# Optimization experiments

Measured on AMD Instinct MI355X. Metric: run time of the kernel, lower is better.

Reference implementation:

```python
import math
import jax, jax.numpy as jnp
from jax import lax
import numpy as np

B, S, D = 4, 128, 256          # batch, image side (l_max = S*S), d_model
FO = 64                        # filter_order (MLP width)
EMB = 3                        # emb_dim (time + 1 band sine/cosine)
FAST, SLOW, TARGET = 0.3, 1.5, 0.01


def setup_inputs() -> dict:
    key = jax.random.key(0)
    ks = jax.random.split(key, 20)
    d3 = 3 * D
    def rn(k, shp, scale):
        return jax.random.normal(k, shp, jnp.float32) * scale
    inp = {
        "x": jax.random.normal(ks[0], (B, S * S, D), jnp.float32),
        # in_proj / out_proj
        "in_w": rn(ks[1], (D, d3), 1.0 / math.sqrt(D)),
        "in_b": jnp.zeros((d3,), jnp.float32),
        "out_w": rn(ks[2], (D, D), 1.0 / math.sqrt(D)),
        "out_b": jnp.zeros((D,), jnp.float32),
        # depthwise 3x3 short filter
        "sf_w": rn(ks[3], (d3, 1, 3, 3), 1.0 / 3.0),
        "sf_b": jnp.zeros((d3,), jnp.float32),
        # Sin activation frequency (shared across all Sin uses; w=1, train_freq=True)
        "freq": jnp.ones((1, FO), jnp.float32),
        # X implicit filter MLP: Linear(3,FO) -> Sin -> Linear(FO,FO) -> Sin -> Linear(FO,FO) -> Sin -> Linear(FO,D,no bias)
        "xw0": rn(ks[4], (EMB, FO), 0.5), "xb0": jnp.zeros((FO,), jnp.float32),
        "xw1": rn(ks[5], (FO, FO), 1.0 / math.sqrt(FO)), "xb1": jnp.zeros((FO,), jnp.float32),
        "xw2": rn(ks[6], (FO, FO), 1.0 / math.sqrt(FO)), "xb2": jnp.zeros((FO,), jnp.float32),
        "xw3": rn(ks[7], (FO, D), 1.0 / math.sqrt(FO)),
        # Y implicit filter MLP (same structure)
        "yw0": rn(ks[8], (EMB, FO), 0.5), "yb0": jnp.zeros((FO,), jnp.float32),
        "yw1": rn(ks[9], (FO, FO), 1.0 / math.sqrt(FO)), "yb1": jnp.zeros((FO,), jnp.float32),
        "yw2": rn(ks[10], (FO, FO), 1.0 / math.sqrt(FO)), "yb2": jnp.zeros((FO,), jnp.float32),
        "yw3": rn(ks[11], (FO, D), 1.0 / math.sqrt(FO)),
        # HyenaFilter2d residual bias D (torch: randn)
        "fbias": jax.random.normal(ks[12], (D,), jnp.float32),
    }
    return inp


def _pos_emb():
    # PositionalEmbedding with emb_dim=3 -> bands=1
    t = jnp.linspace(0.0, 1.0, S)[None, :, None]                 # (1,S,1)
    tr = jnp.linspace(0.0, S - 1.0, S)[None, :, None]
    w_ang = 2.0 * math.pi * tr / S
    f = jnp.linspace(1e-4, 0.0, 1)[None, None]                   # bands=1
    zc = jnp.exp(-1j * f * w_ang)                                # (1,S,1) complex
    z = jnp.concatenate([t, zc.real, zc.imag], axis=-1)          # (1,S,3)
    return z.astype(jnp.float32), t.astype(jnp.float32)


def _decay(t):
    max_d = math.log(TARGET) / FAST
    min_d = math.log(TARGET) / SLOW
    deltas = jnp.linspace(min_d, max_d, D)[None, None]           # (1,1,D) buffer
    return jnp.exp(-t * jnp.abs(deltas))                         # (1,S,D)


def _mlp(z, freq, w0, b0, w1, b1, w2, b2, w3):
    h = jnp.sin(freq * (z @ w0 + b0))
    h = jnp.sin(freq * (h @ w1 + b1))
    h = jnp.sin(freq * (h @ w2 + b2))
    return h @ w3                                                # (1,S,D)


def _fftconv2d(u, k, Db):
    # u: (B,D,S,S), k: (D,S,S), Db: (D,)
    n = 2 * S
    kf = jnp.fft.rfft2(k.astype(jnp.float32), s=(n, n)) / n
    uf = jnp.fft.rfft2(u.astype(jnp.float32), s=(n, n))
    y = jnp.fft.irfft2(uf * kf, s=(n, n))[..., :S, :S]
    return y + u * Db[None, :, None, None]


def reference(x, in_w, in_b, out_w, out_b, sf_w, sf_b, freq,
              xw0, xb0, xw1, xb1, xw2, xb2, xw3,
              yw0, yb0, yw1, yb1, yw2, yb2, yw3, fbias):
    d3 = 3 * D
    # projection and reshape to 2D grid: b (h w) c -> b c h w
    u = x @ in_w + in_b                                          # (B,L,3D)
    u = u.reshape(B, S, S, d3).transpose(0, 3, 1, 2)             # (B,3D,S,S)
    # depthwise 3x3 short filter, padding=2, crop to S (matches Conv padding=2 + [:S])
    uc = lax.conv_general_dilated(u, sf_w, (1, 1), ((2, 2), (2, 2)),
                                  feature_group_count=d3,
                                  dimension_numbers=("NCHW", "OIHW", "NCHW"))
    uc = uc[..., :S, :S] + sf_b[None, :, None, None]
    x0, x1, v = jnp.split(uc, 3, axis=1)                         # each (B,D,S,S)
    # implicit separable 2D filter
    z, t = _pos_emb()
    dec = _decay(t)
    hx = _mlp(z, freq, xw0, xb0, xw1, xb1, xw2, xb2, xw3) * dec  # (1,S,D)
    hy = _mlp(z, freq, yw0, yb0, yw1, yb1, yw2, yb2, yw3) * dec
    k = jnp.einsum('ijk,imk->ijmk', hx, hy)[0]                   # (S,S,D)
    k = jnp.transpose(k, (2, 0, 1))                              # (D,S,S)
    # hyena recurrence (order=2): single gated fft conv
    v = v * x1
    v = _fftconv2d(v, k, fbias)
    y = v * x0
    y = y.transpose(0, 2, 3, 1).reshape(B, S * S, D)             # b c h w -> b (h w) c
    return y @ out_w + out_b
```

## Files before the change

### kernel.cpp

```cpp
#include <hip/hip_runtime.h>
#include <hip/hip_bf16.h>

#define S_DIM 128
#define B_DIM 4
#define L_DIM (S_DIM * S_DIM)

typedef __bf16 bf16x8 __attribute__((ext_vector_type(8)));
typedef float f32x4 __attribute__((ext_vector_type(4)));

__device__ __forceinline__ float b2f(unsigned short u) {
    union { unsigned int i; float f; } v;
    v.i = ((unsigned int)u) << 16;
    return v.f;
}
__device__ __forceinline__ unsigned short f2b(float f) {
    union { float f; unsigned int i; } v;
    v.f = f;
    unsigned int x = v.i;
    return (unsigned short)((x + 0x7FFFu + ((x >> 16) & 1u)) >> 16);
}
__device__ __forceinline__ float ldx(const void* p, size_t i, int f32) {
    return f32 ? ((const float*)p)[i] : b2f(((const unsigned short*)p)[i]);
}

__global__ __launch_bounds__(256) void sniff_dtype(const unsigned short* __restrict__ x,
                                                   int* __restrict__ flag) {
    __shared__ int cnt;
    if (threadIdx.x == 0) cnt = 0;
    __syncthreads();
    int c = 0;
    for (int i = threadIdx.x; i < 32768; i += 256) {
        unsigned int e = (x[i] >> 7) & 0xFFu;
        if (e >= 0x91u) c++;
    }
    atomicAdd(&cnt, c);
    __syncthreads();
    if (threadIdx.x == 0) flag[0] = (cnt > 64) ? 1 : 0;
}

__global__ void transpose_any(const void* __restrict__ src,
                              unsigned short* __restrict__ dst, int R, int C,
                              const int* __restrict__ flag) {
    const int f = flag[0];
    int idx = blockIdx.x * 256 + threadIdx.x;
    if (idx >= R * C) return;
    int r = idx / C, c = idx - r * C;
    dst[c * R + r] = f2b(ldx(src, idx, f));
}

__global__ __launch_bounds__(256) void cast_to_bf16(
    const void* __restrict__ src, size_t s_off,
    unsigned short* __restrict__ dst, size_t n,
    const int* __restrict__ flag)
{
    const int f = flag[0];
    size_t idx = ((size_t)blockIdx.x * 256 + threadIdx.x) * 8;
    const size_t stride = (size_t)gridDim.x * 256 * 8;
    for (; idx < n; idx += stride) {
        if (f) {
            const float4* s4 = (const float4*)((const float*)src + s_off + idx);
            float4 a = s4[0], b = s4[1];
            uint4 w;
            w.x = (unsigned int)f2b(a.x) | ((unsigned int)f2b(a.y) << 16);
            w.y = (unsigned int)f2b(a.z) | ((unsigned int)f2b(a.w) << 16);
            w.z = (unsigned int)f2b(b.x) | ((unsigned int)f2b(b.y) << 16);
            w.w = (unsigned int)f2b(b.z) | ((unsigned int)f2b(b.w) << 16);
            *(uint4*)(dst + idx) = w;
        } else {
            *(uint4*)(dst + idx) =
                *(const uint4*)((const unsigned short*)src + s_off + idx);
        }
    }
}

__global__ __launch_bounds__(256) void filter_mlp(
    const void* __restrict__ freq,
    const void* __restrict__ w0, const void* __restrict__ b0,
    const void* __restrict__ w1, const void* __restrict__ b1,
    const void* __restrict__ w2, const void* __restrict__ b2,
    const void* __restrict__ w3,
    float* __restrict__ out, const int* __restrict__ flag)
{
    __shared__ float hs[64], gs[64];
    const int f32f = flag[0];
    const int s   = blockIdx.x;
    const int tid = threadIdx.x;
    const float t = (float)s / (float)(S_DIM - 1);
    const float ang = 1e-4f * 2.0f * 3.14159265358979323846f * ((float)s / (float)S_DIM);
    const float z0 = t, z1 = cosf(ang), z2 = -sinf(ang);

    if (tid < 64) {
        float fr = ldx(freq, tid, f32f);
        float a = z0 * ldx(w0, 0 * 64 + tid, f32f) + z1 * ldx(w0, 1 * 64 + tid, f32f) +
                  z2 * ldx(w0, 2 * 64 + tid, f32f) + ldx(b0, tid, f32f);
        hs[tid] = sinf(fr * a);
    }
    __syncthreads();
    if (tid < 64) {
        float fr = ldx(freq, tid, f32f);
        float a = ldx(b1, tid, f32f);
        for (int e = 0; e < 64; e++) a += hs[e] * ldx(w1, e * 64 + tid, f32f);
        gs[tid] = sinf(fr * a);
    }
    __syncthreads();
    if (tid < 64) {
        float fr = ldx(freq, tid, f32f);
        float a = ldx(b2, tid, f32f);
        for (int e = 0; e < 64; e++) a += gs[e] * ldx(w2, e * 64 + tid, f32f);
        hs[tid] = sinf(fr * a);
    }
    __syncthreads();
    {
        const float min_d = -3.0701134573253943f;
        const float max_d = -15.350567286626971f;
        float a = 0.f;
        for (int e = 0; e < 64; e++) a += hs[e] * ldx(w3, e * 256 + tid, f32f);
        float delta = min_d + (max_d - min_d) * ((float)tid / 255.0f);
        float dec = expf(-t * fabsf(delta));
        out[s * 256 + tid] = a * dec;
    }
}

__global__ __launch_bounds__(256) void gemm_bt(
    const void* __restrict__ A, size_t a_off, int a_ext,
    const unsigned short* __restrict__ BT,
    const void* __restrict__ bias, int bias_ext,
    void* __restrict__ C, size_t c_off, int c_ext,
    int M, int N, int K, const int* __restrict__ flag)
{
    __shared__ unsigned short As[128 * 40];
    __shared__ unsigned short Bs[128 * 40];

    const int f     = flag[0];
    const int a_f32 = a_ext && f;
    const int b_f32 = bias_ext && f;
    const int c_f32 = c_ext && f;

    const int tid  = threadIdx.x;
    const int m0   = blockIdx.x * 128;
    const int n0   = blockIdx.y * 128;
    const int wid  = tid >> 6;
    const int lane = tid & 63;
    const int lrow = lane & 15;
    const int quad = lane >> 4;
    const int wr   = wid >> 1, wc = wid & 1;

    f32x4 acc[4][4];
#pragma unroll
    for (int a = 0; a < 4; a++)
#pragma unroll
        for (int b = 0; b < 4; b++)
#pragma unroll
            for (int r = 0; r < 4; r++) acc[a][b][r] = 0.0f;

    for (int kc = 0; kc < K; kc += 32) {
#pragma unroll
        for (int h = 0; h < 2; h++) {
            int c    = tid + h * 256;
            int row  = c >> 2;
            int col8 = (c & 3) * 8;
            size_t aidx = a_off + (size_t)(m0 + row) * K + kc + col8;
            if (a_f32) {
                const float4* ga = (const float4*)((const float*)A + aidx);
                float4 p0 = ga[0], p1 = ga[1];
                uint4 w;
                w.x = (unsigned int)f2b(p0.x) | ((unsigned int)f2b(p0.y) << 16);
                w.y = (unsigned int)f2b(p0.z) | ((unsigned int)f2b(p0.w) << 16);
                w.z = (unsigned int)f2b(p1.x) | ((unsigned int)f2b(p1.y) << 16);
                w.w = (unsigned int)f2b(p1.z) | ((unsigned int)f2b(p1.w) << 16);
                *(uint4*)(&As[row * 40 + col8]) = w;
            } else {
                *(uint4*)(&As[row * 40 + col8]) =
                    *(const uint4*)((const unsigned short*)A + aidx);
            }
            *(uint4*)(&Bs[row * 40 + col8]) =
                *(const uint4*)(BT + (size_t)(n0 + row) * K + kc + col8);
        }
        __syncthreads();

        bf16x8 af[4], bfr[4];
#pragma unroll
        for (int fm = 0; fm < 4; fm++)
            af[fm] = *(const bf16x8*)(&As[(wr * 64 + fm * 16 + lrow) * 40 + quad * 8]);
#pragma unroll
        for (int fn = 0; fn < 4; fn++)
            bfr[fn] = *(const bf16x8*)(&Bs[(wc * 64 + fn * 16 + lrow) * 40 + quad * 8]);
#pragma unroll
        for (int fm = 0; fm < 4; fm++)
#pragma unroll
            for (int fn = 0; fn < 4; fn++)
                acc[fm][fn] = __builtin_amdgcn_mfma_f32_16x16x32_bf16(
                    af[fm], bfr[fn], acc[fm][fn], 0, 0, 0);
        __syncthreads();
    }

#pragma unroll
    for (int fm = 0; fm < 4; fm++) {
#pragma unroll
        for (int fn = 0; fn < 4; fn++) {
            int gcol = n0 + wc * 64 + fn * 16 + lrow;
            float bv = ldx(bias, gcol, b_f32);
#pragma unroll
            for (int r = 0; r < 4; r++) {
                int grow = m0 + wr * 64 + fm * 16 + quad * 4 + r;
                size_t cidx = c_off + (size_t)grow * N + gcol;
                float val = acc[fm][fn][r] + bv;
                if (c_f32) ((float*)C)[cidx] = val;
                else       ((unsigned short*)C)[cidx] = f2b(val);
            }
        }
    }
}

__global__ __launch_bounds__(192) void conv3_gate(
    const unsigned short* __restrict__ U, size_t u_zs,
    const void* __restrict__ sfw, const void* __restrict__ sfb,
    unsigned short* __restrict__ Wb, unsigned short* __restrict__ X0, size_t o_zs,
    const int* __restrict__ flag)
{
    __shared__ __align__(16) float x1f[2][256];

    const int f32f = flag[0];
    const int i    = blockIdx.x;
    const int j0   = blockIdx.y * 32;
    const int tid  = threadIdx.x;
    const int wv   = tid >> 6;
    const int lane = tid & 63;
    const int ch0  = wv * 256 + lane * 4;

    const unsigned short* Ub = U + (size_t)blockIdx.z * u_zs;
    unsigned short* Wbb = Wb + (size_t)blockIdx.z * o_zs;
    unsigned short* X0b = X0 + (size_t)blockIdx.z * o_zs;

    float wgt[3][3][4], bias[4];
#pragma unroll
    for (int c = 0; c < 4; c++) {
        int ch = ch0 + c;
        bias[c] = ldx(sfb, ch, f32f);
#pragma unroll
        for (int ki = 0; ki < 3; ki++)
#pragma unroll
            for (int kj = 0; kj < 3; kj++)
                wgt[ki][kj][c] = ldx(sfw, ch * 9 + ki * 3 + kj, f32f);
    }

    bool rok[3];
    const unsigned short* rp[3];
#pragma unroll
    for (int ki = 0; ki < 3; ki++) {
        int row = i + ki - 2;
        rok[ki] = (row >= 0);
        rp[ki]  = Ub + (size_t)(row * S_DIM) * 768 + ch0;
    }

    float win[3][3][4];
#define DLOAD(slot, col)                                                       \
    { _Pragma("unroll") for (int ki = 0; ki < 3; ki++) {                       \
        if (rok[ki] && (col) >= 0) {                                           \
            uint2 p = *(const uint2*)(rp[ki] + (size_t)(col) * 768);           \
            win[slot][ki][0] = b2f((unsigned short)p.x);                       \
            win[slot][ki][1] = b2f((unsigned short)(p.x >> 16));               \
            win[slot][ki][2] = b2f((unsigned short)p.y);                       \
            win[slot][ki][3] = b2f((unsigned short)(p.y >> 16));               \
        } else {                                                               \
            win[slot][ki][0] = 0.f; win[slot][ki][1] = 0.f;                    \
            win[slot][ki][2] = 0.f; win[slot][ki][3] = 0.f;                    \
        } } }

    DLOAD(0, j0 - 2)
    DLOAD(1, j0 - 1)

    uint2 nxt[3];
#pragma unroll
    for (int ki = 0; ki < 3; ki++) {
        uint2 p; p.x = 0u; p.y = 0u;
        if (rok[ki]) p = *(const uint2*)(rp[ki] + (size_t)j0 * 768);
        nxt[ki] = p;
    }

#pragma unroll
    for (int jj = 0; jj < 32; jj++) {
        const int j  = j0 + jj;
        const int sA = jj % 3, sB = (jj + 1) % 3, sC = (jj + 2) % 3;

#pragma unroll
        for (int ki = 0; ki < 3; ki++) {
            win[sC][ki][0] = b2f((unsigned short)nxt[ki].x);
            win[sC][ki][1] = b2f((unsigned short)(nxt[ki].x >> 16));
            win[sC][ki][2] = b2f((unsigned short)nxt[ki].y);
            win[sC][ki][3] = b2f((unsigned short)(nxt[ki].y >> 16));
        }
        {
            const int jn = j + 1;
            const bool jok = (jn < S_DIM);
#pragma unroll
            for (int ki = 0; ki < 3; ki++) {
                uint2 p; p.x = 0u; p.y = 0u;
                if (jok && rok[ki]) p = *(const uint2*)(rp[ki] + (size_t)jn * 768);
                nxt[ki] = p;
            }
        }

        float o[4];
#pragma unroll
        for (int c = 0; c < 4; c++) {
            float a = bias[c];
#pragma unroll
            for (int ki = 0; ki < 3; ki++)
                a += wgt[ki][0][c] * win[sA][ki][c]
                   + wgt[ki][1][c] * win[sB][ki][c]
                   + wgt[ki][2][c] * win[sC][ki][c];
            o[c] = a;
        }

        const size_t oidx = (size_t)(i * S_DIM + j) * 256 + lane * 4;
        if (wv == 1) {
            float4 v4; v4.x = o[0]; v4.y = o[1]; v4.z = o[2]; v4.w = o[3];
            *(float4*)(&x1f[jj & 1][lane * 4]) = v4;
        } else if (wv == 0) {
            unsigned int lo = (unsigned int)f2b(o[0]) | ((unsigned int)f2b(o[1]) << 16);
            unsigned int hi = (unsigned int)f2b(o[2]) | ((unsigned int)f2b(o[3]) << 16);
            uint2 st; st.x = lo; st.y = hi;
            *(uint2*)(&X0b[oidx]) = st;
        }
        __syncthreads();
        if (wv == 2) {
            float4 xp = *(const float4*)(&x1f[jj & 1][lane * 4]);
            float r0 = o[0] * xp.x;
            float r1 = o[1] * xp.y;
            float r2 = o[2] * xp.z;
            float r3 = o[3] * xp.w;
            unsigned int lo = (unsigned int)f2b(r0) | ((unsigned int)f2b(r1) << 16);
            unsigned int hi = (unsigned int)f2b(r2) | ((unsigned int)f2b(r3) << 16);
            uint2 st; st.x = lo; st.y = hi;
            *(uint2*)(&Wbb[oidx]) = st;
        }
    }
#undef DLOAD
}

__global__ __launch_bounds__(256) void conv_j(
    const unsigned short* __restrict__ Wb, size_t zs,
    const float* __restrict__ hy,
    unsigned short* __restrict__ Aout)
{
    const int i = blockIdx.x;
    const int h = blockIdx.y;
    const int d = threadIdx.x;
    const size_t zoff = (size_t)blockIdx.z * zs;
    const size_t sbase = zoff + (size_t)(i * S_DIM) * 256;
    const unsigned short* Wp = Wb + sbase + d;
    const float* hyd = hy + d;

    for (int pick = 0; pick < 2; pick++) {
        const int jt = pick ? (7 - h) : h;
        const int j0 = jt * 16;
        float acc[16];
#pragma unroll
        for (int jj = 0; jj < 16; jj++) acc[jj] = 0.f;

        float Wn[19];
#pragma unroll
        for (int t = 0; t < 19; t++) {
            int r = j0 - 3 + t;
            Wn[t] = (r >= 0) ? b2f(Wp[(size_t)r * 256]) : 0.f;
        }
        const int qmax = j0 + 15;
        float hvA[4], hvB[4];
#pragma unroll
        for (int idx = 0; idx < 4; idx++) hvA[idx] = hyd[idx * 256];

        for (int q0 = 0; q0 <= qmax; q0 += 8) {
#pragma unroll
            for (int idx = 0; idx < 4; idx++) hvB[idx] = hyd[(q0 + 4 + idx) * 256];
#pragma unroll
            for (int idx = 0; idx < 4; idx++)
#pragma unroll
                for (int jj = 0; jj < 16; jj++)
                    acc[jj] += hvA[idx] * Wn[jj + 3 - idx];
#pragma unroll
            for (int t = 18; t >= 4; t--) Wn[t] = Wn[t - 4];
#pragma unroll
            for (int t = 0; t < 4; t++) {
                int r = j0 - q0 - 7 + t;
                Wn[t] = (r >= 0) ? b2f(Wp[(size_t)r * 256]) : 0.f;
            }
            if (q0 + 8 <= qmax) {
#pragma unroll
                for (int idx = 0; idx < 4; idx++) hvA[idx] = hyd[(q0 + 8 + idx) * 256];
            }
#pragma unroll
            for (int idx = 0; idx < 4; idx++)
#pragma unroll
                for (int jj = 0; jj < 16; jj++)
                    acc[jj] += hvB[idx] * Wn[jj + 3 - idx];
            if (q0 + 8 <= qmax) {
#pragma unroll
                for (int t = 18; t >= 4; t--) Wn[t] = Wn[t - 4];
#pragma unroll
                for (int t = 0; t < 4; t++) {
                    int r = j0 - q0 - 11 + t;
                    Wn[t] = (r >= 0) ? b2f(Wp[(size_t)r * 256]) : 0.f;
                }
            }
        }
#pragma unroll
        for (int jj = 0; jj < 16; jj++)
            Aout[sbase + (size_t)(j0 + jj) * 256 + d] = f2b(acc[jj]);
    }
}

__global__ __launch_bounds__(256) void conv_i(
    const unsigned short* __restrict__ Ain, size_t zs,
    const float* __restrict__ hx,
    const unsigned short* __restrict__ Wb,
    const unsigned short* __restrict__ X0,
    const void* __restrict__ fbias,
    unsigned short* __restrict__ Gout,
    const int* __restrict__ flag)
{
    const int f32f = flag[0];
    const int j = blockIdx.x;
    const int h = blockIdx.y;
    const int d = threadIdx.x;
    const size_t zoff = (size_t)blockIdx.z * zs;
    const unsigned short* Ap = Ain + zoff + (size_t)j * 256 + d;
    const float* hxd = hx + d;
    const float fb = ldx(fbias, d, f32f);

    for (int pick = 0; pick < 2; pick++) {
        const int it = pick ? (7 - h) : h;
        const int i0 = it * 16;
        float acc[16];
#pragma unroll
        for (int ii = 0; ii < 16; ii++) acc[ii] = 0.f;

        float Wn[19];
#pragma unroll
        for (int t = 0; t < 19; t++) {
            int r = i0 - 3 + t;
            Wn[t] = (r >= 0) ? b2f(Ap[(size_t)r * (S_DIM * 256)]) : 0.f;
        }
        const int qmax = i0 + 15;
        float hvA[4], hvB[4];
#pragma unroll
        for (int idx = 0; idx < 4; idx++) hvA[idx] = hxd[idx * 256];

        for (int q0 = 0; q0 <= qmax; q0 += 8) {
#pragma unroll
            for (int idx = 0; idx < 4; idx++) hvB[idx] = hxd[(q0 + 4 + idx) * 256];
#pragma unroll
            for (int idx = 0; idx < 4; idx++)
#pragma unroll
                for (int ii = 0; ii < 16; ii++)
                    acc[ii] += hvA[idx] * Wn[ii + 3 - idx];
#pragma unroll
            for (int t = 18; t >= 4; t--) Wn[t] = Wn[t - 4];
#pragma unroll
            for (int t = 0; t < 4; t++) {
                int r = i0 - q0 - 7 + t;
                Wn[t] = (r >= 0) ? b2f(Ap[(size_t)r * (S_DIM * 256)]) : 0.f;
            }
            if (q0 + 8 <= qmax) {
#pragma unroll
                for (int idx = 0; idx < 4; idx++) hvA[idx] = hxd[(q0 + 8 + idx) * 256];
            }
#pragma unroll
            for (int idx = 0; idx < 4; idx++)
#pragma unroll
                for (int ii = 0; ii < 16; ii++)
                    acc[ii] += hvB[idx] * Wn[ii + 3 - idx];
            if (q0 + 8 <= qmax) {
#pragma unroll
                for (int t = 18; t >= 4; t--) Wn[t] = Wn[t - 4];
#pragma unroll
                for (int t = 0; t < 4; t++) {
                    int r = i0 - q0 - 11 + t;
                    Wn[t] = (r >= 0) ? b2f(Ap[(size_t)r * (S_DIM * 256)]) : 0.f;
                }
            }
        }
#pragma unroll
        for (int ii = 0; ii < 16; ii++) {
            int i = i0 + ii;
            size_t idx = zoff + (size_t)(i * S_DIM + j) * 256 + d;
            float wv  = b2f(Wb[idx]);
            float x0v = b2f(X0[idx]);
            float y = acc[ii] * (1.0f / 256.0f) + wv * fb;
            Gout[idx] = f2b(y * x0v);
        }
    }
}

extern "C" void kernel_launch(void* const* d_in, const int* in_sizes, int n_in,
                              void* d_out, int out_size, void* d_ws, size_t ws_size,
                              hipStream_t stream)
{
    const void* x     = d_in[0];
    const void* in_w  = d_in[1];
    const void* in_b  = d_in[2];
    const void* out_w = d_in[3];
    const void* out_b_= d_in[4];
    const void* sf_w  = d_in[5];
    const void* sf_b  = d_in[6];
    const void* freq  = d_in[7];
    const void* xw0 = d_in[8];  const void* xb0 = d_in[9];
    const void* xw1 = d_in[10]; const void* xb1 = d_in[11];
    const void* xw2 = d_in[12]; const void* xb2 = d_in[13];
    const void* xw3 = d_in[14];
    const void* yw0 = d_in[15]; const void* yb0 = d_in[16];
    const void* yw1 = d_in[17]; const void* yb1 = d_in[18];
    const void* yw2 = d_in[19]; const void* yb2 = d_in[20];
    const void* yw3 = d_in[21];
    const void* fbias = d_in[22];

    char* ws = (char*)d_ws;
    const size_t UZ  = (size_t)L_DIM * 768;
    const size_t OZ  = (size_t)L_DIM * 256;

    const size_t need_fused = 168558608;
    bool fused = (ws_size >= need_fused);

    if (fused) {
        unsigned short* u_f  = (unsigned short*)(ws + 0);
        unsigned short* A_f  = (unsigned short*)(ws + 0);
        unsigned short* G_f  = (unsigned short*)(ws + 33554432);
        unsigned short* Wb_f = (unsigned short*)(ws + 100663296);
        unsigned short* X0_f = (unsigned short*)(ws + 134217728);
        unsigned short* xb_f = (unsigned short*)(ws + 100663296);
        float* hx            = (float*)(ws + 167772160);
        float* hy            = (float*)(ws + 167903232);
        unsigned short* tin  = (unsigned short*)(ws + 168034304);
        unsigned short* tout = (unsigned short*)(ws + 168427520);
        int* flag            = (int*)(ws + 168558592);

        sniff_dtype<<<1, 256, 0, stream>>>((const unsigned short*)x, flag);
        transpose_any<<<dim3(768), 256, 0, stream>>>(in_w, tin, 256, 768, flag);
        transpose_any<<<dim3(256), 256, 0, stream>>>(out_w, tout, 256, 256, flag);
        filter_mlp<<<dim3(S_DIM), 256, 0, stream>>>(freq, xw0, xb0, xw1, xb1, xw2, xb2, xw3, hx, flag);
        filter_mlp<<<dim3(S_DIM), 256, 0, stream>>>(freq, yw0, yb0, yw1, yb1, yw2, yb2, yw3, hy, flag);

        cast_to_bf16<<<dim3(2048), 256, 0, stream>>>(
            x, 0, xb_f, (size_t)B_DIM * L_DIM * 256, flag);
        gemm_bt<<<dim3(512, 6), 256, 0, stream>>>(
            xb_f, 0, 0, tin, in_b, 1, u_f, 0, 0, B_DIM * L_DIM, 768, 256, flag);
        conv3_gate<<<dim3(S_DIM, 4, B_DIM), 192, 0, stream>>>(
            u_f, UZ, sf_w, sf_b, Wb_f, X0_f, OZ, flag);
        conv_j<<<dim3(S_DIM, 4, B_DIM), 256, 0, stream>>>(Wb_f, OZ, hy, A_f);
        conv_i<<<dim3(S_DIM, 4, B_DIM), 256, 0, stream>>>(
            A_f, OZ, hx, Wb_f, X0_f, fbias, G_f, flag);
        gemm_bt<<<dim3(512, 2), 256, 0, stream>>>(
            G_f, 0, 0, tout, out_b_, 1, d_out, 0, 1, B_DIM * L_DIM, 256, 256, flag);
    } else {
        unsigned short* u_b  = (unsigned short*)(ws + 0);
        unsigned short* A_b  = (unsigned short*)(ws + 0);
        unsigned short* G_b  = (unsigned short*)(ws + 8388608);
        unsigned short* Wb_b = (unsigned short*)(ws + 25165824);
        unsigned short* X0_b = (unsigned short*)(ws + 33554432);
        unsigned short* xb_b = (unsigned short*)(ws + 25165824);
        float* hx            = (float*)(ws + 41943040);
        float* hy            = (float*)(ws + 42074112);
        unsigned short* tin  = (unsigned short*)(ws + 42205184);
        unsigned short* tout = (unsigned short*)(ws + 42598400);
        int* flag            = (int*)(ws + 42729472);

        sniff_dtype<<<1, 256, 0, stream>>>((const unsigned short*)x, flag);
        transpose_any<<<dim3(768), 256, 0, stream>>>(in_w, tin, 256, 768, flag);
        transpose_any<<<dim3(256), 256, 0, stream>>>(out_w, tout, 256, 256, flag);
        filter_mlp<<<dim3(S_DIM), 256, 0, stream>>>(freq, xw0, xb0, xw1, xb1, xw2, xb2, xw3, hx, flag);
        filter_mlp<<<dim3(S_DIM), 256, 0, stream>>>(freq, yw0, yb0, yw1, yb1, yw2, yb2, yw3, hy, flag);

        for (int b = 0; b < B_DIM; b++) {
            size_t xoff = (size_t)b * OZ;
            cast_to_bf16<<<dim3(2048), 256, 0, stream>>>(
                x, xoff, xb_b, (size_t)L_DIM * 256, flag);
            gemm_bt<<<dim3(128, 6), 256, 0, stream>>>(
                xb_b, 0, 0, tin, in_b, 1, u_b, 0, 0, L_DIM, 768, 256, flag);
            conv3_gate<<<dim3(S_DIM, 4, 1), 192, 0, stream>>>(
                u_b, 0, sf_w, sf_b, Wb_b, X0_b, 0, flag);
            conv_j<<<dim3(S_DIM, 4, 1), 256, 0, stream>>>(Wb_b, 0, hy, A_b);
            conv_i<<<dim3(S_DIM, 4, 1), 256, 0, stream>>>(
                A_b, 0, hx, Wb_b, X0_b, fbias, G_b, flag);
            gemm_bt<<<dim3(128, 2), 256, 0, stream>>>(
                G_b, 0, 0, tout, out_b_, 1, d_out, xoff, 1, L_DIM, 256, 256, flag);
        }
    }
}
```

Baseline: 603.7 us.

## Process two rows per thread in separable convs and fuse input cast into GEMM

conv_j and conv_i now compute two adjacent rows/columns per thread, so each loaded filter tap (hy/hx) is reused twice and the grid is halved. The separate cast_to_bf16 pass is removed, and the first GEMM reads x directly with a flag that presumably handles dtype conversion on load. This removes one full read/write of the activation tensor and halves filter-tap loads, at the cost of doubled register pressure (two accumulator and window arrays) and fewer blocks in flight.

Result: slower. 680.7 us (+12.8%).

```diff
diff --git a/kernel.cpp b/kernel.cpp
--- a/kernel.cpp
+++ b/kernel.cpp
@@ -46,31 +46,6 @@
     if (idx >= R * C) return;
     int r = idx / C, c = idx - r * C;
     dst[c * R + r] = f2b(ldx(src, idx, f));
-}
-
-__global__ __launch_bounds__(256) void cast_to_bf16(
-    const void* __restrict__ src, size_t s_off,
-    unsigned short* __restrict__ dst, size_t n,
-    const int* __restrict__ flag)
-{
-    const int f = flag[0];
-    size_t idx = ((size_t)blockIdx.x * 256 + threadIdx.x) * 8;
-    const size_t stride = (size_t)gridDim.x * 256 * 8;
-    for (; idx < n; idx += stride) {
-        if (f) {
-            const float4* s4 = (const float4*)((const float*)src + s_off + idx);
-            float4 a = s4[0], b = s4[1];
-            uint4 w;
-            w.x = (unsigned int)f2b(a.x) | ((unsigned int)f2b(a.y) << 16);
-            w.y = (unsigned int)f2b(a.z) | ((unsigned int)f2b(a.w) << 16);
-            w.z = (unsigned int)f2b(b.x) | ((unsigned int)f2b(b.y) << 16);
-            w.w = (unsigned int)f2b(b.z) | ((unsigned int)f2b(b.w) << 16);
-            *(uint4*)(dst + idx) = w;
-        } else {
-            *(uint4*)(dst + idx) =
-                *(const uint4*)((const unsigned short*)src + s_off + idx);
-        }
-    }
 }
 
 __global__ __launch_bounds__(256) void filter_mlp(
@@ -344,69 +319,84 @@
     const float* __restrict__ hy,
     unsigned short* __restrict__ Aout)
 {
-    const int i = blockIdx.x;
-    const int h = blockIdx.y;
-    const int d = threadIdx.x;
+    const int ip = blockIdx.x;
+    const int h  = blockIdx.y;
+    const int d  = threadIdx.x;
     const size_t zoff = (size_t)blockIdx.z * zs;
-    const size_t sbase = zoff + (size_t)(i * S_DIM) * 256;
-    const unsigned short* Wp = Wb + sbase + d;
+    const size_t sb0 = zoff + (size_t)((2 * ip) * S_DIM) * 256;
+    const size_t sb1 = sb0 + (size_t)S_DIM * 256;
+    const unsigned short* W0 = Wb + sb0 + d;
+    const unsigned short* W1 = Wb + sb1 + d;
     const float* hyd = hy + d;
 
     for (int pick = 0; pick < 2; pick++) {
         const int jt = pick ? (7 - h) : h;
         const int j0 = jt * 16;
-        float acc[16];
-#pragma unroll
-        for (int jj = 0; jj < 16; jj++) acc[jj] = 0.f;
-
-        float Wn[19];
+        float a0[16], a1[16];
+#pragma unroll
+        for (int jj = 0; jj < 16; jj++) { a0[jj] = 0.f; a1[jj] = 0.f; }
+
+        float Wn0[19], Wn1[19];
 #pragma unroll
         for (int t = 0; t < 19; t++) {
             int r = j0 - 3 + t;
-            Wn[t] = (r >= 0) ? b2f(Wp[(size_t)r * 256]) : 0.f;
-        }
-        const int qmax = j0 + 15;
+            bool ok = (r >= 0);
+            Wn0[t] = ok ? b2f(W0[(size_t)r * 256]) : 0.f;
+            Wn1[t] = ok ? b2f(W1[(size_t)r * 256]) : 0.f;
+        }
         float hvA[4], hvB[4];
 #pragma unroll
         for (int idx = 0; idx < 4; idx++) hvA[idx] = hyd[idx * 256];
 
-        for (int q0 = 0; q0 <= qmax; q0 += 8) {
+        const int niter = (j0 + 16) >> 3;
+        for (int it = 0; it < niter; it++) {
+            const int q0 = it * 8;
 #pragma unroll
             for (int idx = 0; idx < 4; idx++) hvB[idx] = hyd[(q0 + 4 + idx) * 256];
 #pragma unroll
             for (int idx = 0; idx < 4; idx++)
 #pragma unroll
-                for (int jj = 0; jj < 16; jj++)
-                    acc[jj] += hvA[idx] * Wn[jj + 3 - idx];
-#pragma unroll
-            for (int t = 18; t >= 4; t--) Wn[t] = Wn[t - 4];
+                for (int jj = 0; jj < 16; jj++) {
+                    a0[jj] += hvA[idx] * Wn0[jj + 3 - idx];
+                    a1[jj] += hvA[idx] * Wn1[jj + 3 - idx];
+                }
+#pragma unroll
+            for (int t = 18; t >= 4; t--) { Wn0[t] = Wn0[t - 4]; Wn1[t] = Wn1[t - 4]; }
 #pragma unroll
             for (int t = 0; t < 4; t++) {
                 int r = j0 - q0 - 7 + t;
-                Wn[t] = (r >= 0) ? b2f(Wp[(size_t)r * 256]) : 0.f;
-            }
-            if (q0 + 8 <= qmax) {
+                bool ok = (r >= 0);
+                Wn0[t] = ok ? b2f(W0[(size_t)r * 256]) : 0.f;
+                Wn1[t] = ok ? b2f(W1[(size_t)r * 256]) : 0.f;
+            }
+            if (it + 1 < niter) {
 #pragma unroll
                 for (int idx = 0; idx < 4; idx++) hvA[idx] = hyd[(q0 + 8 + idx) * 256];
             }
 #pragma unroll
             for (int idx = 0; idx < 4; idx++)
 #pragma unroll
-                for (int jj = 0; jj < 16; jj++)
-                    acc[jj] += hvB[idx] * Wn[jj + 3 - idx];
-            if (q0 + 8 <= qmax) {
-#pragma unroll
-                for (int t = 18; t >= 4; t--) Wn[t] = Wn[t - 4];
+                for (int jj = 0; jj < 16; jj++) {
+                    a0[jj] += hvB[idx] * Wn0[jj + 3 - idx];
+                    a1[jj] += hvB[idx] * Wn1[jj + 3 - idx];
+                }
+            if (it + 1 < niter) {
+#pragma unroll
+                for (int t = 18; t >= 4; t--) { Wn0[t] = Wn0[t - 4]; Wn1[t] = Wn1[t - 4]; }
 #pragma unroll
                 for (int t = 0; t < 4; t++) {
                     int r = j0 - q0 - 11 + t;
-                    Wn[t] = (r >= 0) ? b2f(Wp[(size_t)r * 256]) : 0.f;
+                    bool ok = (r >= 0);
+                    Wn0[t] = ok ? b2f(W0[(size_t)r * 256]) : 0.f;
+                    Wn1[t] = ok ? b2f(W1[(size_t)r * 256]) : 0.f;
                 }
             }
         }
 #pragma unroll
-        for (int jj = 0; jj < 16; jj++)
-            Aout[sbase + (size_t)(j0 + jj) * 256 + d] = f2b(acc[jj]);
+        for (int jj = 0; jj < 16; jj++) {
+            Aout[sb0 + (size_t)(j0 + jj) * 256 + d] = f2b(a0[jj]);
+            Aout[sb1 + (size_t)(j0 + jj) * 256 + d] = f2b(a1[jj]);
+        }
     }
 }
 
@@ -420,74 +410,92 @@
     const int* __restrict__ flag)
 {
     const int f32f = flag[0];
-    const int j = blockIdx.x;
-    const int h = blockIdx.y;
-    const int d = threadIdx.x;
+    const int jx = blockIdx.x;
+    const int h  = blockIdx.y;
+    const int d  = threadIdx.x;
     const size_t zoff = (size_t)blockIdx.z * zs;
-    const unsigned short* Ap = Ain + zoff + (size_t)j * 256 + d;
+    const int jc0 = 2 * jx;
+    const unsigned short* A0 = Ain + zoff + (size_t)jc0 * 256 + d;
+    const unsigned short* A1 = A0 + 256;
     const float* hxd = hx + d;
     const float fb = ldx(fbias, d, f32f);
 
     for (int pick = 0; pick < 2; pick++) {
-        const int it = pick ? (7 - h) : h;
-        const int i0 = it * 16;
-        float acc[16];
-#pragma unroll
-        for (int ii = 0; ii < 16; ii++) acc[ii] = 0.f;
-
-        float Wn[19];
+        const int it0 = pick ? (7 - h) : h;
+        const int i0 = it0 * 16;
+        float a0[16], a1[16];
+#pragma unroll
+        for (int ii = 0; ii < 16; ii++) { a0[ii] = 0.f; a1[ii] = 0.f; }
+
+        float Wn0[19], Wn1[19];
 #pragma unroll
         for (int t = 0; t < 19; t++) {
             int r = i0 - 3 + t;
-            Wn[t] = (r >= 0) ? b2f(Ap[(size_t)r * (S_DIM * 256)]) : 0.f;
-        }
-        const int qmax = i0 + 15;
+            bool ok = (r >= 0);
+            Wn0[t] = ok ? b2f(A0[(size_t)r * (S_DIM * 256)]) : 0.f;
+            Wn1[t] = ok ? b2f(A1[(size_t)r * (S_DIM * 256)]) : 0.f;
+        }
         float hvA[4], hvB[4];
 #pragma unroll
         for (int idx = 0; idx < 4; idx++) hvA[idx] = hxd[idx * 256];
 
-        for (int q0 = 0; q0 <= qmax; q0 += 8) {
+        const int niter = (i0 + 16) >> 3;
+        for (int itq = 0; itq < niter; itq++) {
+            const int q0 = itq * 8;
 #pragma unroll
             for (int idx = 0; idx < 4; idx++) hvB[idx] = hxd[(q0 + 4 + idx) * 256];
 #pragma unroll
             for (int idx = 0; idx < 4; idx++)
 #pragma unroll
-                for (int ii = 0; ii < 16; ii++)
-                    acc[ii] += hvA[idx] * Wn[ii + 3 - idx];
-#pragma unroll
-            for (int t = 18; t >= 4; t--) Wn[t] = Wn[t - 4];
+                for (int ii = 0; ii < 16; ii++) {
+                    a0[ii] += hvA[idx] * Wn0[ii + 3 - idx];
+                    a1[ii] += hvA[idx] * Wn1[ii + 3 - idx];
+                }
+#pragma unroll
+            for (int t = 18; t >= 4; t--) { Wn0[t] = Wn0[t - 4]; Wn1[t] = Wn1[t - 4]; }
 #pragma unroll
             for (int t = 0; t < 4; t++) {
                 int r = i0 - q0 - 7 + t;
-                Wn[t] = (r >= 0) ? b2f(Ap[(size_t)r * (S_DIM * 256)]) : 0.f;
-            }
-            if (q0 + 8 <= qmax) {
+                bool ok = (r >= 0);
+                Wn0[t] = ok ? b2f(A0[(size_t)r * (S_DIM * 256)]) : 0.f;
+                Wn1[t] = ok ? b2f(A1[(size_t)r * (S_DIM * 256)]) : 0.f;
+            }
+            if (itq + 1 < niter) {
 #pragma unroll
                 for (int idx = 0; idx < 4; idx++) hvA[idx] = hxd[(q0 + 8 + idx) * 256];
             }
 #pragma unroll
             for (int idx = 0; idx < 4; idx++)
 #pragma unroll
-                for (int ii = 0; ii < 16; ii++)
-                    acc[ii] += hvB[idx] * Wn[ii + 3 - idx];
-            if (q0 + 8 <= qmax) {
-#pragma unroll
-                for (int t = 18; t >= 4; t--) Wn[t] = Wn[t - 4];
+                for (int ii = 0; ii < 16; ii++) {
+                    a0[ii] += hvB[idx] * Wn0[ii + 3 - idx];
+                    a1[ii] += hvB[idx] * Wn1[ii + 3 - idx];
+                }
+            if (itq + 1 < niter) {
+#pragma unroll
+                for (int t = 18; t >= 4; t--) { Wn0[t] = Wn0[t - 4]; Wn1[t] = Wn1[t - 4]; }
 #pragma unroll
                 for (int t = 0; t < 4; t++) {
                     int r = i0 - q0 - 11 + t;
-                    Wn[t] = (r >= 0) ? b2f(Ap[(size_t)r * (S_DIM * 256)]) : 0.f;
+                    bool ok = (r >= 0);
+                    Wn0[t] = ok ? b2f(A0[(size_t)r * (S_DIM * 256)]) : 0.f;
+                    Wn1[t] = ok ? b2f(A1[(size_t)r * (S_DIM * 256)]) : 0.f;
                 }
             }
         }
 #pragma unroll
         for (int ii = 0; ii < 16; ii++) {
             int i = i0 + ii;
-            size_t idx = zoff + (size_t)(i * S_DIM + j) * 256 + d;
-            float wv  = b2f(Wb[idx]);
-            float x0v = b2f(X0[idx]);
-            float y = acc[ii] * (1.0f / 256.0f) + wv * fb;
-            Gout[idx] = f2b(y * x0v);
+            size_t idx0 = zoff + (size_t)(i * S_DIM + jc0) * 256 + d;
+            size_t idx1 = idx0 + 256;
+            float wv0  = b2f(Wb[idx0]);
+            float x00  = b2f(X0[idx0]);
+            float wv1  = b2f(Wb[idx1]);
+            float x01  = b2f(X0[idx1]);
+            float y0 = a0[ii] * (1.0f / 256.0f) + wv0 * fb;
+            float y1 = a1[ii] * (1.0f / 256.0f) + wv1 * fb;
+            Gout[idx0] = f2b(y0 * x00);
+            Gout[idx1] = f2b(y1 * x01);
         }
     }
 }
@@ -527,7 +535,6 @@
         unsigned short* G_f  = (unsigned short*)(ws + 33554432);
         unsigned short* Wb_f = (unsigned short*)(ws + 100663296);
         unsigned short* X0_f = (unsigned short*)(ws + 134217728);
-        unsigned short* xb_f = (unsigned short*)(ws + 100663296);
         float* hx            = (float*)(ws + 167772160);
         float* hy            = (float*)(ws + 167903232);
         unsigned short* tin  = (unsigned short*)(ws + 168034304);
@@ -540,14 +547,12 @@
         filter_mlp<<<dim3(S_DIM), 256, 0, stream>>>(freq, xw0, xb0, xw1, xb1, xw2, xb2, xw3, hx, flag);
         filter_mlp<<<dim3(S_DIM), 256, 0, stream>>>(freq, yw0, yb0, yw1, yb1, yw2, yb2, yw3, hy, flag);
 
-        cast_to_bf16<<<dim3(2048), 256, 0, stream>>>(
-            x, 0, xb_f, (size_t)B_DIM * L_DIM * 256, flag);
         gemm_bt<<<dim3(512, 6), 256, 0, stream>>>(
-            xb_f, 0, 0, tin, in_b, 1, u_f, 0, 0, B_DIM * L_DIM, 768, 256, flag);
+            x, 0, 1, tin, in_b, 1, u_f, 0, 0, B_DIM * L_DIM, 768, 256, flag);
         conv3_gate<<<dim3(S_DIM, 4, B_DIM), 192, 0, stream>>>(
             u_f, UZ, sf_w, sf_b, Wb_f, X0_f, OZ, flag);
-        conv_j<<<dim3(S_DIM, 4, B_DIM), 256, 0, stream>>>(Wb_f, OZ, hy, A_f);
-        conv_i<<<dim3(S_DIM, 4, B_DIM), 256, 0, stream>>>(
+        conv_j<<<dim3(S_DIM / 2, 4, B_DIM), 256, 0, stream>>>(Wb_f, OZ, hy, A_f);
+        conv_i<<<dim3(S_DIM / 2, 4, B_DIM), 256, 0, stream>>>(
             A_f, OZ, hx, Wb_f, X0_f, fbias, G_f, flag);
         gemm_bt<<<dim3(512, 2), 256, 0, stream>>>(
             G_f, 0, 0, tout, out_b_, 1, d_out, 0, 1, B_DIM * L_DIM, 256, 256, flag);
@@ -557,7 +562,6 @@
         unsigned short* G_b  = (unsigned short*)(ws + 8388608);
         unsigned short* Wb_b = (unsigned short*)(ws + 25165824);
         unsigned short* X0_b = (unsigned short*)(ws + 33554432);
-        unsigned short* xb_b = (unsigned short*)(ws + 25165824);
         float* hx            = (float*)(ws + 41943040);
         float* hy            = (float*)(ws + 42074112);
         unsigned short* tin  = (unsigned short*)(ws + 42205184);
@@ -572,14 +576,12 @@
 
         for (int b = 0; b < B_DIM; b++) {
             size_t xoff = (size_t)b * OZ;
-            cast_to_bf16<<<dim3(2048), 256, 0, stream>>>(
-                x, xoff, xb_b, (size_t)L_DIM * 256, flag);
             gemm_bt<<<dim3(128, 6), 256, 0, stream>>>(
-                xb_b, 0, 0, tin, in_b, 1, u_b, 0, 0, L_DIM, 768, 256, flag);
+                x, xoff, 1, tin, in_b, 1, u_b, 0, 0, L_DIM, 768, 256, flag);
             conv3_gate<<<dim3(S_DIM, 4, 1), 192, 0, stream>>>(
                 u_b, 0, sf_w, sf_b, Wb_b, X0_b, 0, flag);
-            conv_j<<<dim3(S_DIM, 4, 1), 256, 0, stream>>>(Wb_b, 0, hy, A_b);
-            conv_i<<<dim3(S_DIM, 4, 1), 256, 0, stream>>>(
+            conv_j<<<dim3(S_DIM / 2, 4, 1), 256, 0, stream>>>(Wb_b, 0, hy, A_b);
+            conv_i<<<dim3(S_DIM / 2, 4, 1), 256, 0, stream>>>(
                 A_b, 0, hx, Wb_b, X0_b, fbias, G_b, flag);
             gemm_bt<<<dim3(128, 2), 256, 0, stream>>>(
                 G_b, 0, 0, tout, out_b_, 1, d_out, xoff, 1, L_DIM, 256, 256, flag);
```
